# Kernel optimization log

Measured on AMD Instinct MI355X. Metric: run time of the kernel, lower is better.

The kernel has to match this reference:

```python
import jax, jax.numpy as jnp
import numpy as np

DIM = 1024
NUM_SKILLS = 50


def setup_inputs() -> dict:
    key = jax.random.key(0)
    ks = jax.random.split(key, 7)
    n_tokens = 4096
    scale = 1.0 / np.sqrt(DIM)
    x = jax.random.normal(ks[0], (n_tokens, DIM), dtype=jnp.float32)
    # Stacked expert weights: skill i is Linear(dim,dim) -> ReLU -> Linear(dim,dim)
    W1 = jax.random.uniform(ks[1], (NUM_SKILLS, DIM, DIM), jnp.float32, -scale, scale)
    b1 = jax.random.uniform(ks[2], (NUM_SKILLS, DIM), jnp.float32, -scale, scale)
    W2 = jax.random.uniform(ks[3], (NUM_SKILLS, DIM, DIM), jnp.float32, -scale, scale)
    b2 = jax.random.uniform(ks[4], (NUM_SKILLS, DIM), jnp.float32, -scale, scale)
    # Gating linear: Linear(dim, num_skills)
    Wg = jax.random.uniform(ks[5], (DIM, NUM_SKILLS), jnp.float32, -scale, scale)
    bg = jax.random.uniform(ks[6], (NUM_SKILLS,), jnp.float32, -scale, scale)
    return {"x": x, "W1": W1, "b1": b1, "W2": W2, "b2": b2, "Wg": Wg, "bg": bg}


def reference(x, W1, b1, W2, b2, Wg, bg):
    # Soft-MoE path (skill_id=None): softmax gate over all experts,
    # every expert applied to every token, weighted sum.
    gates = jax.nn.softmax(x @ Wg + bg, axis=-1)            # [n, E]
    h = jax.nn.relu(jnp.einsum('nd,edh->neh', x, W1) + b1)  # [n, E, d]
    y = jnp.einsum('neh,ehd->ned', h, W2) + b2              # [n, E, d]
    out = jnp.einsum('ned,ne->nd', y, gates)                # [n, d]
    return out
```

## Files before the change

kernel.cpp:

```cpp
#include <hip/hip_runtime.h>
#include <stdint.h>

#define AS1 __attribute__((address_space(1)))
#define AS3 __attribute__((address_space(3)))

typedef unsigned short u16;
typedef __attribute__((ext_vector_type(8))) short s16x8;
typedef __attribute__((ext_vector_type(8))) unsigned short u16x8;
typedef __attribute__((ext_vector_type(4))) float f32x4;

__device__ __forceinline__ u16 f2bf(float f) {
    union { float f; unsigned int u; } v; v.f = f;
    unsigned int r = v.u + 0x7fffu + ((v.u >> 16) & 1u);
    return (u16)(r >> 16);
}

__device__ __forceinline__ void gld_lds16(const u16* g, u16* l) {
    __builtin_amdgcn_global_load_lds((AS1 unsigned int*)(uintptr_t)g,
                                     (AS3 unsigned int*)(uintptr_t)l, 16, 0, 0);
}

__global__ void convert_x_kernel(const float* __restrict__ X, u16* __restrict__ Xb, int total8) {
    int i = blockIdx.x * 256 + threadIdx.x;
    if (i < total8) {
        f32x4 a = ((const f32x4*)X)[2 * i];
        f32x4 b = ((const f32x4*)X)[2 * i + 1];
        u16x8 o;
#pragma unroll
        for (int j = 0; j < 4; j++) { o[j] = f2bf(a[j]); o[4 + j] = f2bf(b[j]); }
        ((u16x8*)Xb)[i] = o;
    }
}

__global__ void gate_kernel(const float* __restrict__ X, const float* __restrict__ Wg,
                            const float* __restrict__ bg, float* __restrict__ gates, int nt) {
    __shared__ float xs[1024];
    const int n = blockIdx.x;
    const int t = threadIdx.x;
#pragma unroll
    for (int i = 0; i < 16; i++) xs[t + i * 64] = X[(size_t)n * 1024 + t + i * 64];
    __syncthreads();
    float a = -INFINITY;
    if (t < 50) {
        float s0 = 0.f, s1 = 0.f, s2 = 0.f, s3 = 0.f;
        for (int d = 0; d < 1024; d += 4) {
            s0 += xs[d + 0] * Wg[(d + 0) * 50 + t];
            s1 += xs[d + 1] * Wg[(d + 1) * 50 + t];
            s2 += xs[d + 2] * Wg[(d + 2) * 50 + t];
            s3 += xs[d + 3] * Wg[(d + 3) * 50 + t];
        }
        a = (s0 + s1) + (s2 + s3) + bg[t];
    }
    float m = a;
#pragma unroll
    for (int off = 32; off > 0; off >>= 1) m = fmaxf(m, __shfl_xor(m, off));
    float p = (t < 50) ? __expf(a - m) : 0.f;
    float ss = p;
#pragma unroll
    for (int off = 32; off > 0; off >>= 1) ss += __shfl_xor(ss, off);
    if (t < 50) gates[(size_t)n * 50 + t] = p / ss;
}

__global__ void transpose_kernel(const float* __restrict__ W1s, const float* __restrict__ W2s,
                                 u16* __restrict__ Wt1, u16* __restrict__ Wt2, int eg) {
    __shared__ u16 tile[64 * 65];
    const int t = threadIdx.x;
    const int z = blockIdx.z;
    const float* src; u16* dst;
    if (z < eg) { src = W1s + ((size_t)z << 20); dst = Wt1 + ((size_t)z << 20); }
    else        { src = W2s + ((size_t)(z - eg) << 20); dst = Wt2 + ((size_t)(z - eg) << 20); }
    const int k0 = blockIdx.y * 64;
    const int n0 = blockIdx.x * 64;
#pragma unroll
    for (int p = 0; p < 4; p++) {
        int r = (t >> 4) + 16 * p;
        int c = t & 15;
        f32x4 v = *(const f32x4*)(src + (size_t)(k0 + r) * 1024 + n0 + c * 4);
#pragma unroll
        for (int j = 0; j < 4; j++) tile[r * 65 + c * 4 + j] = f2bf(v[j]);
    }
    __syncthreads();
#pragma unroll
    for (int p = 0; p < 2; p++) {
        int h = (t >> 3) + 32 * p;
        int c = t & 7;
        u16x8 o;
#pragma unroll
        for (int j = 0; j < 8; j++) o[j] = tile[(c * 8 + j) * 65 + h];
        *(u16x8*)(dst + (size_t)(n0 + h) * 1024 + k0 + c * 8) = o;
    }
}

#define CT_STRIDE 136
__global__ __launch_bounds__(256, 3)
void gemm1_kernel(const u16* __restrict__ X, const u16* __restrict__ Wt1,
                  const float* __restrict__ b1, const float* __restrict__ gates,
                  u16* __restrict__ Hp, int nt, int egbase) {
    __shared__ __align__(16) u16 smem[128 * CT_STRIDE];
    u16* Asm = smem;
    u16* Bsm = smem + 128 * 64;
    const int tid = threadIdx.x, wave = tid >> 6, lane = tid & 63;
    const int e = blockIdx.z;
    const int n0 = blockIdx.x * 128, m0 = blockIdx.y * 128;
    const int lr = lane >> 3, lc = lane & 7, cg = lc ^ lr;

    const u16* Ag = X + (size_t)(m0 + wave * 32 + lr) * 1024 + cg * 8;
    const u16* Bg = Wt1 + ((size_t)e << 20) + (size_t)(n0 + wave * 32 + lr) * 1024 + cg * 8;
    u16* Al = Asm + (wave * 32) * 64;
    u16* Bl = Bsm + (wave * 32) * 64;

    const int wm = wave & 1, wn = wave >> 1;
    const int fr = lane & 15, fq = lane >> 4;
    int aoff[2][4], boff[2][4];
#pragma unroll
    for (int kk = 0; kk < 2; ++kk)
#pragma unroll
        for (int i = 0; i < 4; ++i) {
            int ra = wm * 64 + i * 16 + fr;
            int rb = wn * 64 + i * 16 + fr;
            aoff[kk][i] = ra * 64 + (((kk * 4 + fq) ^ (ra & 7)) * 8);
            boff[kk][i] = rb * 64 + (((kk * 4 + fq) ^ (rb & 7)) * 8);
        }

    f32x4 acc[16];
#pragma unroll
    for (int i = 0; i < 16; i++) acc[i] = (f32x4){0.f, 0.f, 0.f, 0.f};

    for (int kt = 0; kt < 1024; kt += 64) {
        __syncthreads();
#pragma unroll
        for (int i = 0; i < 4; ++i) {
            gld_lds16(Ag + kt + (size_t)(i * 8) * 1024, Al + (i * 8) * 64);
            gld_lds16(Bg + kt + (size_t)(i * 8) * 1024, Bl + (i * 8) * 64);
        }
        __syncthreads();
#pragma unroll
        for (int kk = 0; kk < 2; ++kk) {
            s16x8 av[4], bv[4];
#pragma unroll
            for (int i = 0; i < 4; i++) av[i] = *(const s16x8*)(Asm + aoff[kk][i]);
#pragma unroll
            for (int i = 0; i < 4; i++) bv[i] = *(const s16x8*)(Bsm + boff[kk][i]);
#pragma unroll
            for (int mi = 0; mi < 4; mi++)
#pragma unroll
                for (int nj = 0; nj < 4; nj++)
                    acc[mi * 4 + nj] =
                        __builtin_amdgcn_mfma_f32_16x16x32_bf16(av[mi], bv[nj], acc[mi * 4 + nj], 0, 0, 0);
        }
    }

    const float* b1e = b1 + (size_t)e * 1024;
    float b1v[4];
#pragma unroll
    for (int nj = 0; nj < 4; nj++) b1v[nj] = b1e[n0 + wn * 64 + nj * 16 + fr];
    const int eglob = egbase + e;
    float gv[4][4];
#pragma unroll
    for (int mi = 0; mi < 4; mi++)
#pragma unroll
        for (int ri = 0; ri < 4; ri++)
            gv[mi][ri] = gates[(size_t)(m0 + wm * 64 + mi * 16 + fq * 4 + ri) * 50 + eglob];

    __syncthreads();
#pragma unroll
    for (int mi = 0; mi < 4; mi++) {
#pragma unroll
        for (int ri = 0; ri < 4; ri++) {
            int row = wm * 64 + mi * 16 + fq * 4 + ri;
#pragma unroll
            for (int nj = 0; nj < 4; nj++) {
                int col = wn * 64 + nj * 16 + fr;
                float h = acc[mi * 4 + nj][ri] + b1v[nj];
                h = h > 0.f ? h * gv[mi][ri] : 0.f;
                smem[row * CT_STRIDE + col] = f2bf(h);
            }
        }
    }
    __syncthreads();
    u16* HpE = Hp + (size_t)e * nt * 1024;
    const int c = tid & 15, rb = tid >> 4;
#pragma unroll
    for (int p = 0; p < 8; p++) {
        int r = rb + p * 16;
        u16x8 v = *(const u16x8*)(smem + r * CT_STRIDE + c * 8);
        *(u16x8*)(HpE + (size_t)(m0 + r) * 1024 + n0 + c * 8) = v;
    }
}

__global__ __launch_bounds__(256, 3)
void gemm2_kernel(const u16* __restrict__ Hp, const u16* __restrict__ Wt2,
                  float* __restrict__ partial, int nt, int eg, int init) {
    __shared__ __align__(16) u16 Asm[128 * 64];
    __shared__ __align__(16) u16 Bsm[128 * 64];
    const int tid = threadIdx.x, wave = tid >> 6, lane = tid & 63;
    const int s = blockIdx.z;
    const int n0 = blockIdx.x * 128, m0 = blockIdx.y * 128;
    const int lr = lane >> 3, lc = lane & 7, cg = lc ^ lr;

    const u16* Agr = Hp + (size_t)(m0 + wave * 32 + lr) * 1024 + cg * 8;
    const u16* Bgr = Wt2 + (size_t)(n0 + wave * 32 + lr) * 1024 + cg * 8;
    u16* Al = Asm + (wave * 32) * 64;
    u16* Bl = Bsm + (wave * 32) * 64;

    const int wm = wave & 1, wn = wave >> 1;
    const int fr = lane & 15, fq = lane >> 4;
    int aoff[2][4], boff[2][4];
#pragma unroll
    for (int kk = 0; kk < 2; ++kk)
#pragma unroll
        for (int i = 0; i < 4; ++i) {
            int ra = wm * 64 + i * 16 + fr;
            int rb = wn * 64 + i * 16 + fr;
            aoff[kk][i] = ra * 64 + (((kk * 4 + fq) ^ (ra & 7)) * 8);
            boff[kk][i] = rb * 64 + (((kk * 4 + fq) ^ (rb & 7)) * 8);
        }

    f32x4 acc[16];
#pragma unroll
    for (int i = 0; i < 16; i++) acc[i] = (f32x4){0.f, 0.f, 0.f, 0.f};

    const int Kg2 = eg * 512;
    for (int kt = s * Kg2; kt < (s + 1) * Kg2; kt += 64) {
        const int e = kt >> 10;
        const int k = kt & 1023;
        const u16* Ag = Agr + (size_t)e * nt * 1024 + k;
        const u16* Bg = Bgr + ((size_t)e << 20) + k;
        __syncthreads();
#pragma unroll
        for (int i = 0; i < 4; ++i) {
            gld_lds16(Ag + (size_t)(i * 8) * 1024, Al + (i * 8) * 64);
            gld_lds16(Bg + (size_t)(i * 8) * 1024, Bl + (i * 8) * 64);
        }
        __syncthreads();
#pragma unroll
        for (int kk = 0; kk < 2; ++kk) {
            s16x8 av[4], bv[4];
#pragma unroll
            for (int i = 0; i < 4; i++) av[i] = *(const s16x8*)(Asm + aoff[kk][i]);
#pragma unroll
            for (int i = 0; i < 4; i++) bv[i] = *(const s16x8*)(Bsm + boff[kk][i]);
#pragma unroll
            for (int mi = 0; mi < 4; mi++)
#pragma unroll
                for (int nj = 0; nj < 4; nj++)
                    acc[mi * 4 + nj] =
                        __builtin_amdgcn_mfma_f32_16x16x32_bf16(av[mi], bv[nj], acc[mi * 4 + nj], 0, 0, 0);
        }
    }

    float* pp = partial + (size_t)s * nt * 1024;
#pragma unroll
    for (int mi = 0; mi < 4; mi++) {
#pragma unroll
        for (int ri = 0; ri < 4; ri++) {
            int gr = m0 + wm * 64 + mi * 16 + fq * 4 + ri;
#pragma unroll
            for (int nj = 0; nj < 4; nj++) {
                size_t idx = (size_t)gr * 1024 + n0 + wn * 64 + nj * 16 + fr;
                float v = acc[mi * 4 + nj][ri];
                if (!init) v += pp[idx];
                pp[idx] = v;
            }
        }
    }
}

__global__ void finalize_kernel(const float* __restrict__ partial, const float* __restrict__ gates,
                                const float* __restrict__ b2, float* __restrict__ out, int nt) {
    __shared__ float gs[50];
    const int n = blockIdx.x;
    const int t = threadIdx.x;
    if (t < 50) gs[t] = gates[(size_t)n * 50 + t];
    __syncthreads();
    const size_t base = (size_t)n * 1024;
    const size_t stride = (size_t)nt * 1024;
#pragma unroll
    for (int i = 0; i < 4; i++) {
        int d = t + i * 256;
        float v = partial[base + d] + partial[stride + base + d];
#pragma unroll 10
        for (int e2 = 0; e2 < 50; e2++) v += gs[e2] * b2[e2 * 1024 + d];
        out[base + d] = v;
    }
}

extern "C" void kernel_launch(void* const* d_in, const int* in_sizes, int n_in,
                              void* d_out, int out_size, void* d_ws, size_t ws_size,
                              hipStream_t stream) {
    const float* x  = (const float*)d_in[0];
    const float* W1 = (const float*)d_in[1];
    const float* b1 = (const float*)d_in[2];
    const float* W2 = (const float*)d_in[3];
    const float* b2 = (const float*)d_in[4];
    const float* Wg = (const float*)d_in[5];
    const float* bg = (const float*)d_in[6];
    float* out = (float*)d_out;
    const int nt = in_sizes[0] / 1024;

    char* w = (char*)d_ws;
    auto carve = [&](size_t bytes) -> char* {
        char* p = w; w += (bytes + 255) & ~(size_t)255; return p;
    };
    float* gates   = (float*)carve((size_t)nt * 50 * 4);
    float* partial = (float*)carve((size_t)2 * nt * 1024 * 4);
    u16*   xb      = (u16*)carve((size_t)nt * 1024 * 2);
    const size_t fixed = (size_t)(w - (char*)d_ws);

    int eg = 1;
    const int cand[6] = {50, 25, 10, 5, 2, 1};
    for (int i = 0; i < 6; i++) {
        size_t need = fixed + (size_t)cand[i] * ((size_t)2 * 2097152 + (size_t)nt * 1024 * 2) + 4096;
        if (need <= ws_size) { eg = cand[i]; break; }
    }
    u16* Wt1 = (u16*)carve((size_t)eg * 1048576 * 2);
    u16* Wt2 = (u16*)carve((size_t)eg * 1048576 * 2);
    u16* Hp  = (u16*)carve((size_t)eg * nt * 1024 * 2);

    convert_x_kernel<<<(nt * 1024 / 8 + 255) / 256, 256, 0, stream>>>(x, xb, nt * 1024 / 8);
    gate_kernel<<<nt, 64, 0, stream>>>(x, Wg, bg, gates, nt);

    const int groups = 50 / eg;
    for (int g = 0; g < groups; ++g) {
        transpose_kernel<<<dim3(16, 16, 2 * eg), 256, 0, stream>>>(
            W1 + ((size_t)(g * eg) << 20), W2 + ((size_t)(g * eg) << 20), Wt1, Wt2, eg);
        gemm1_kernel<<<dim3(8, nt / 128, eg), 256, 0, stream>>>(
            xb, Wt1, b1 + (size_t)g * eg * 1024, gates, Hp, nt, g * eg);
        gemm2_kernel<<<dim3(8, nt / 128, 2), 256, 0, stream>>>(
            Hp, Wt2, partial, nt, eg, g == 0 ? 1 : 0);
    }
    finalize_kernel<<<nt, 256, 0, stream>>>(partial, gates, b2, out, nt);
}
```

Baseline: 1.625 ms.

## Use 256x256 tiles with 4-stage LDS pipeline and split-K of four in GEMMs

```diff
diff --git a/kernel.cpp b/kernel.cpp
--- a/kernel.cpp
+++ b/kernel.cpp
@@ -91,170 +91,159 @@
     }
 }
 
-#define CT_STRIDE 136
-__global__ __launch_bounds__(256, 3)
+
+#define BUF_U16 16384
+
+#define STG1(t) { int bo = ((t) & 3) * BUF_U16;                                   \
+        const u16* a = Ag + (t) * 32; const u16* b = Bg + (t) * 32;               \
+        gld_lds16(a, Ald + bo);          gld_lds16(a + 131072, Ald + bo + 4096);  \
+        gld_lds16(b, Bld + bo);          gld_lds16(b + 131072, Bld + bo + 4096); }
+
+#define STG2(t) { int kt = kb + (t) * 32; int ee = kt >> 10; int kk = kt & 1023;  \
+        const u16* a = Agr + (size_t)ee * ntk + kk;                               \
+        const u16* b = Bgr + ((size_t)ee << 20) + kk;                             \
+        int bo = ((t) & 3) * BUF_U16;                                             \
+        gld_lds16(a, Ald + bo);          gld_lds16(a + 131072, Ald + bo + 4096);  \
+        gld_lds16(b, Bld + bo);          gld_lds16(b + 131072, Bld + bo + 4096); }
+
+#define MMSTEP(t, VM, DO, STG) {                                                  \
+        asm volatile("s_waitcnt vmcnt(" VM ")\n\ts_barrier" ::: "memory");        \
+        if (DO) STG((t) + 3);                                                     \
+        const u16* bp = smem + ((t) & 3) * BUF_U16;                               \
+        s16x8 av[8], bv[4];                                                       \
+        _Pragma("unroll") for (int mi = 0; mi < 8; mi++)                          \
+            av[mi] = *(const s16x8*)(bp + aoff[mi]);                              \
+        _Pragma("unroll") for (int nj = 0; nj < 4; nj++)                          \
+            bv[nj] = *(const s16x8*)(bp + boff[nj]);                              \
+        __builtin_amdgcn_s_setprio(1);                                            \
+        _Pragma("unroll") for (int mi = 0; mi < 8; mi++)                          \
+        _Pragma("unroll") for (int nj = 0; nj < 4; nj++)                          \
+            acc[mi * 4 + nj] = __builtin_amdgcn_mfma_f32_16x16x32_bf16(           \
+                av[mi], bv[nj], acc[mi * 4 + nj], 0, 0, 0);                       \
+        __builtin_amdgcn_s_setprio(0); }
+
+__global__ __launch_bounds__(512, 2)
 void gemm1_kernel(const u16* __restrict__ X, const u16* __restrict__ Wt1,
                   const float* __restrict__ b1, const float* __restrict__ gates,
                   u16* __restrict__ Hp, int nt, int egbase) {
-    __shared__ __align__(16) u16 smem[128 * CT_STRIDE];
-    u16* Asm = smem;
-    u16* Bsm = smem + 128 * 64;
+    __shared__ __align__(16) u16 smem[67584];
     const int tid = threadIdx.x, wave = tid >> 6, lane = tid & 63;
     const int e = blockIdx.z;
-    const int n0 = blockIdx.x * 128, m0 = blockIdx.y * 128;
-    const int lr = lane >> 3, lc = lane & 7, cg = lc ^ lr;
-
-    const u16* Ag = X + (size_t)(m0 + wave * 32 + lr) * 1024 + cg * 8;
-    const u16* Bg = Wt1 + ((size_t)e << 20) + (size_t)(n0 + wave * 32 + lr) * 1024 + cg * 8;
-    u16* Al = Asm + (wave * 32) * 64;
-    u16* Bl = Bsm + (wave * 32) * 64;
-
-    const int wm = wave & 1, wn = wave >> 1;
+    const int n0 = blockIdx.x * 256, m0 = blockIdx.y * 256;
+
+    const int srow = wave * 16 + (lane >> 2);
+    const int scg = ((lane & 3) ^ (srow & 3)) * 8;
+    const u16* Ag = X + (size_t)(m0 + srow) * 1024 + scg;
+    const u16* Bg = Wt1 + ((size_t)e << 20) + (size_t)(n0 + srow) * 1024 + scg;
+    u16* Ald = smem + wave * 512;
+    u16* Bld = smem + 8192 + wave * 512;
+
+    const int wm = wave >> 2, wn = wave & 3;
     const int fr = lane & 15, fq = lane >> 4;
-    int aoff[2][4], boff[2][4];
-#pragma unroll
-    for (int kk = 0; kk < 2; ++kk)
-#pragma unroll
-        for (int i = 0; i < 4; ++i) {
-            int ra = wm * 64 + i * 16 + fr;
-            int rb = wn * 64 + i * 16 + fr;
-            aoff[kk][i] = ra * 64 + (((kk * 4 + fq) ^ (ra & 7)) * 8);
-            boff[kk][i] = rb * 64 + (((kk * 4 + fq) ^ (rb & 7)) * 8);
-        }
-
-    f32x4 acc[16];
-#pragma unroll
-    for (int i = 0; i < 16; i++) acc[i] = (f32x4){0.f, 0.f, 0.f, 0.f};
-
-    for (int kt = 0; kt < 1024; kt += 64) {
-        __syncthreads();
-#pragma unroll
-        for (int i = 0; i < 4; ++i) {
-            gld_lds16(Ag + kt + (size_t)(i * 8) * 1024, Al + (i * 8) * 64);
-            gld_lds16(Bg + kt + (size_t)(i * 8) * 1024, Bl + (i * 8) * 64);
-        }
-        __syncthreads();
-#pragma unroll
-        for (int kk = 0; kk < 2; ++kk) {
-            s16x8 av[4], bv[4];
-#pragma unroll
-            for (int i = 0; i < 4; i++) av[i] = *(const s16x8*)(Asm + aoff[kk][i]);
-#pragma unroll
-            for (int i = 0; i < 4; i++) bv[i] = *(const s16x8*)(Bsm + boff[kk][i]);
-#pragma unroll
-            for (int mi = 0; mi < 4; mi++)
-#pragma unroll
-                for (int nj = 0; nj < 4; nj++)
-                    acc[mi * 4 + nj] =
-                        __builtin_amdgcn_mfma_f32_16x16x32_bf16(av[mi], bv[nj], acc[mi * 4 + nj], 0, 0, 0);
-        }
-    }
+    int aoff[8], boff[4];
+#pragma unroll
+    for (int mi = 0; mi < 8; mi++) {
+        int ra = wm * 128 + mi * 16 + fr;
+        aoff[mi] = ra * 32 + ((fq ^ (ra & 3)) * 8);
+    }
+#pragma unroll
+    for (int nj = 0; nj < 4; nj++) {
+        int rb = wn * 64 + nj * 16 + fr;
+        boff[nj] = 8192 + rb * 32 + ((fq ^ (rb & 3)) * 8);
+    }
+
+    f32x4 acc[32];
+#pragma unroll
+    for (int i = 0; i < 32; i++) acc[i] = (f32x4){0.f, 0.f, 0.f, 0.f};
+
+    STG1(0); STG1(1); STG1(2);
+    for (int t = 0; t < 29; ++t) MMSTEP(t, "8", 1, STG1);
+    MMSTEP(29, "8", 0, STG1);
+    MMSTEP(30, "4", 0, STG1);
+    MMSTEP(31, "0", 0, STG1);
 
     const float* b1e = b1 + (size_t)e * 1024;
     float b1v[4];
 #pragma unroll
     for (int nj = 0; nj < 4; nj++) b1v[nj] = b1e[n0 + wn * 64 + nj * 16 + fr];
     const int eglob = egbase + e;
-    float gv[4][4];
-#pragma unroll
-    for (int mi = 0; mi < 4; mi++)
-#pragma unroll
-        for (int ri = 0; ri < 4; ri++)
-            gv[mi][ri] = gates[(size_t)(m0 + wm * 64 + mi * 16 + fq * 4 + ri) * 50 + eglob];
-
-    __syncthreads();
-#pragma unroll
-    for (int mi = 0; mi < 4; mi++) {
+
+    __syncthreads();
+#pragma unroll
+    for (int mi = 0; mi < 8; mi++) {
 #pragma unroll
         for (int ri = 0; ri < 4; ri++) {
-            int row = wm * 64 + mi * 16 + fq * 4 + ri;
+            int row = wm * 128 + mi * 16 + fq * 4 + ri;
+            float g = gates[(size_t)(m0 + row) * 50 + eglob];
 #pragma unroll
             for (int nj = 0; nj < 4; nj++) {
                 int col = wn * 64 + nj * 16 + fr;
                 float h = acc[mi * 4 + nj][ri] + b1v[nj];
-                h = h > 0.f ? h * gv[mi][ri] : 0.f;
-                smem[row * CT_STRIDE + col] = f2bf(h);
+                h = h > 0.f ? h * g : 0.f;
+                smem[row * 264 + col] = f2bf(h);
             }
         }
     }
     __syncthreads();
     u16* HpE = Hp + (size_t)e * nt * 1024;
-    const int c = tid & 15, rb = tid >> 4;
-#pragma unroll
-    for (int p = 0; p < 8; p++) {
-        int r = rb + p * 16;
-        u16x8 v = *(const u16x8*)(smem + r * CT_STRIDE + c * 8);
+    const int c = tid & 31, rr = tid >> 5;
+#pragma unroll
+    for (int p = 0; p < 16; p++) {
+        int r = rr + p * 16;
+        u16x8 v = *(const u16x8*)(smem + r * 264 + c * 8);
         *(u16x8*)(HpE + (size_t)(m0 + r) * 1024 + n0 + c * 8) = v;
     }
 }
 
-__global__ __launch_bounds__(256, 3)
+__global__ __launch_bounds__(512, 2)
 void gemm2_kernel(const u16* __restrict__ Hp, const u16* __restrict__ Wt2,
                   float* __restrict__ partial, int nt, int eg, int init) {
-    __shared__ __align__(16) u16 Asm[128 * 64];
-    __shared__ __align__(16) u16 Bsm[128 * 64];
+    __shared__ __align__(16) u16 smem[65536];
     const int tid = threadIdx.x, wave = tid >> 6, lane = tid & 63;
     const int s = blockIdx.z;
-    const int n0 = blockIdx.x * 128, m0 = blockIdx.y * 128;
-    const int lr = lane >> 3, lc = lane & 7, cg = lc ^ lr;
-
-    const u16* Agr = Hp + (size_t)(m0 + wave * 32 + lr) * 1024 + cg * 8;
-    const u16* Bgr = Wt2 + (size_t)(n0 + wave * 32 + lr) * 1024 + cg * 8;
-    u16* Al = Asm + (wave * 32) * 64;
-    u16* Bl = Bsm + (wave * 32) * 64;
-
-    const int wm = wave & 1, wn = wave >> 1;
+    const int n0 = blockIdx.x * 256, m0 = blockIdx.y * 256;
+
+    const int srow = wave * 16 + (lane >> 2);
+    const int scg = ((lane & 3) ^ (srow & 3)) * 8;
+    const u16* Agr = Hp + (size_t)(m0 + srow) * 1024 + scg;
+    const u16* Bgr = Wt2 + (size_t)(n0 + srow) * 1024 + scg;
+    const size_t ntk = (size_t)nt * 1024;
+    u16* Ald = smem + wave * 512;
+    u16* Bld = smem + 8192 + wave * 512;
+
+    const int wm = wave >> 2, wn = wave & 3;
     const int fr = lane & 15, fq = lane >> 4;
-    int aoff[2][4], boff[2][4];
-#pragma unroll
-    for (int kk = 0; kk < 2; ++kk)
-#pragma unroll
-        for (int i = 0; i < 4; ++i) {
-            int ra = wm * 64 + i * 16 + fr;
-            int rb = wn * 64 + i * 16 + fr;
-            aoff[kk][i] = ra * 64 + (((kk * 4 + fq) ^ (ra & 7)) * 8);
-            boff[kk][i] = rb * 64 + (((kk * 4 + fq) ^ (rb & 7)) * 8);
-        }
-
-    f32x4 acc[16];
-#pragma unroll
-    for (int i = 0; i < 16; i++) acc[i] = (f32x4){0.f, 0.f, 0.f, 0.f};
-
-    const int Kg2 = eg * 512;
-    for (int kt = s * Kg2; kt < (s + 1) * Kg2; kt += 64) {
-        const int e = kt >> 10;
-        const int k = kt & 1023;
-        const u16* Ag = Agr + (size_t)e * nt * 1024 + k;
-        const u16* Bg = Bgr + ((size_t)e << 20) + k;
-        __syncthreads();
-#pragma unroll
-        for (int i = 0; i < 4; ++i) {
-            gld_lds16(Ag + (size_t)(i * 8) * 1024, Al + (i * 8) * 64);
-            gld_lds16(Bg + (size_t)(i * 8) * 1024, Bl + (i * 8) * 64);
-        }
-        __syncthreads();
-#pragma unroll
-        for (int kk = 0; kk < 2; ++kk) {
-            s16x8 av[4], bv[4];
-#pragma unroll
-            for (int i = 0; i < 4; i++) av[i] = *(const s16x8*)(Asm + aoff[kk][i]);
-#pragma unroll
-            for (int i = 0; i < 4; i++) bv[i] = *(const s16x8*)(Bsm + boff[kk][i]);
-#pragma unroll
-            for (int mi = 0; mi < 4; mi++)
-#pragma unroll
-                for (int nj = 0; nj < 4; nj++)
-                    acc[mi * 4 + nj] =
-                        __builtin_amdgcn_mfma_f32_16x16x32_bf16(av[mi], bv[nj], acc[mi * 4 + nj], 0, 0, 0);
-        }
-    }
+    int aoff[8], boff[4];
+#pragma unroll
+    for (int mi = 0; mi < 8; mi++) {
+        int ra = wm * 128 + mi * 16 + fr;
+        aoff[mi] = ra * 32 + ((fq ^ (ra & 3)) * 8);
+    }
+#pragma unroll
+    for (int nj = 0; nj < 4; nj++) {
+        int rb = wn * 64 + nj * 16 + fr;
+        boff[nj] = 8192 + rb * 32 + ((fq ^ (rb & 3)) * 8);
+    }
+
+    f32x4 acc[32];
+#pragma unroll
+    for (int i = 0; i < 32; i++) acc[i] = (f32x4){0.f, 0.f, 0.f, 0.f};
+
+    const int NT = eg * 8;
+    const int kb = s * NT * 32;
+
+    STG2(0); STG2(1); STG2(2);
+    for (int t = 0; t < NT - 3; ++t) MMSTEP(t, "8", 1, STG2);
+    MMSTEP(NT - 3, "8", 0, STG2);
+    MMSTEP(NT - 2, "4", 0, STG2);
+    MMSTEP(NT - 1, "0", 0, STG2);
 
     float* pp = partial + (size_t)s * nt * 1024;
 #pragma unroll
-    for (int mi = 0; mi < 4; mi++) {
+    for (int mi = 0; mi < 8; mi++) {
 #pragma unroll
         for (int ri = 0; ri < 4; ri++) {
-            int gr = m0 + wm * 64 + mi * 16 + fq * 4 + ri;
+            int gr = m0 + wm * 128 + mi * 16 + fq * 4 + ri;
 #pragma unroll
             for (int nj = 0; nj < 4; nj++) {
                 size_t idx = (size_t)gr * 1024 + n0 + wn * 64 + nj * 16 + fr;
@@ -274,11 +263,12 @@
     if (t < 50) gs[t] = gates[(size_t)n * 50 + t];
     __syncthreads();
     const size_t base = (size_t)n * 1024;
-    const size_t stride = (size_t)nt * 1024;
+    const size_t st = (size_t)nt * 1024;
 #pragma unroll
     for (int i = 0; i < 4; i++) {
         int d = t + i * 256;
-        float v = partial[base + d] + partial[stride + base + d];
+        float v = partial[base + d] + partial[st + base + d]
+                + partial[2 * st + base + d] + partial[3 * st + base + d];
 #pragma unroll 10
         for (int e2 = 0; e2 < 50; e2++) v += gs[e2] * b2[e2 * 1024 + d];
         out[base + d] = v;
@@ -303,7 +293,7 @@
         char* p = w; w += (bytes + 255) & ~(size_t)255; return p;
     };
     float* gates   = (float*)carve((size_t)nt * 50 * 4);
-    float* partial = (float*)carve((size_t)2 * nt * 1024 * 4);
+    float* partial = (float*)carve((size_t)4 * nt * 1024 * 4);
     u16*   xb      = (u16*)carve((size_t)nt * 1024 * 2);
     const size_t fixed = (size_t)(w - (char*)d_ws);
 
@@ -324,9 +314,9 @@
     for (int g = 0; g < groups; ++g) {
         transpose_kernel<<<dim3(16, 16, 2 * eg), 256, 0, stream>>>(
             W1 + ((size_t)(g * eg) << 20), W2 + ((size_t)(g * eg) << 20), Wt1, Wt2, eg);
-        gemm1_kernel<<<dim3(8, nt / 128, eg), 256, 0, stream>>>(
+        gemm1_kernel<<<dim3(4, nt / 256, eg), 512, 0, stream>>>(
             xb, Wt1, b1 + (size_t)g * eg * 1024, gates, Hp, nt, g * eg);
-        gemm2_kernel<<<dim3(8, nt / 128, 2), 256, 0, stream>>>(
+        gemm2_kernel<<<dim3(4, nt / 256, 4), 512, 0, stream>>>(
             Hp, Wt2, partial, nt, eg, g == 0 ? 1 : 0);
     }
     finalize_kernel<<<nt, 256, 0, stream>>>(partial, gates, b2, out, nt);
```

Result: faster. 1.422 ms (-12.5%).
